# Kernel tuning notes

Hardware: AMD Instinct MI355X
Metric: run time of the kernel (lower is better)

The kernel has to match this reference:

```python
import jax, jax.numpy as jnp
import numpy as np
import math

NUM_BUCKETS = 32
MAX_DISTANCE = 128


def _relative_position_bucket(relative_position):
    # Unidirectional (bidirectional=False): rp = max(-relative_position, 0)
    rp = jnp.maximum(-relative_position, 0)
    max_exact = NUM_BUCKETS // 2  # 16
    is_small = rp < max_exact
    rp_f = jnp.maximum(rp, 1).astype(jnp.float32)
    large = max_exact + (
        jnp.log(rp_f / max_exact) / math.log(MAX_DISTANCE / max_exact)
        * (NUM_BUCKETS - max_exact)
    ).astype(jnp.int32)
    large = jnp.minimum(large, NUM_BUCKETS - 1)
    return jnp.where(is_small, rp, large)


def _t5_rel_bias(bias_table, T):
    # bias_table: [num_buckets, n_heads] -> [1, n_heads, T, T]
    ctx = jnp.arange(T, dtype=jnp.int32)[:, None]
    mem = jnp.arange(T, dtype=jnp.int32)[None, :]
    buckets = _relative_position_bucket(mem - ctx)  # [T, T]
    values = bias_table[buckets]  # [T, T, H]
    return jnp.transpose(values, (2, 0, 1))[None]  # [1, H, T, T]


def setup_inputs() -> dict:
    key = jax.random.key(0)
    ks = jax.random.split(key, 6)
    B, T, C, H = 2, 2048, 1024, 16
    x = jax.random.normal(ks[0], (B, T, C), dtype=jnp.float32)
    W_attn = jax.random.normal(ks[1], (C, 3 * C), dtype=jnp.float32) * 0.02
    b_attn = jnp.zeros((3 * C,), dtype=jnp.float32)
    W_proj = jax.random.normal(ks[2], (C, C), dtype=jnp.float32) * 0.02
    b_proj = jnp.zeros((C,), dtype=jnp.float32)
    bias_table = jax.random.normal(ks[3], (NUM_BUCKETS, H), dtype=jnp.float32) * 0.02
    return {"x": x, "W_attn": W_attn, "b_attn": b_attn,
            "W_proj": W_proj, "b_proj": b_proj, "bias_table": bias_table}


def reference(x, W_attn, b_attn, W_proj, b_proj, bias_table):
    B, T, C = x.shape
    H = bias_table.shape[1]
    D = C // H
    qkv = x @ W_attn + b_attn  # [B, T, 3C]
    q, k, v = jnp.split(qkv, 3, axis=-1)
    # [B, T, C] -> [B, H, T, D]
    q = q.reshape(B, T, H, D).transpose(0, 2, 1, 3)
    k = k.reshape(B, T, H, D).transpose(0, 2, 1, 3)
    v = v.reshape(B, T, H, D).transpose(0, 2, 1, 3)
    rel_bias = _t5_rel_bias(bias_table, T)  # [1, H, T, T]
    att = jnp.einsum('bhtd,bhsd->bhts', q, k) * (1.0 / math.sqrt(D))
    att = att + rel_bias
    causal = jnp.tril(jnp.ones((T, T), dtype=bool))
    att = jnp.where(causal, att, -jnp.inf)
    att = jax.nn.softmax(att, axis=-1)
    y = jnp.einsum('bhts,bhsd->bhtd', att, v)  # [B, H, T, D]
    y = y.transpose(0, 2, 1, 3).reshape(B, T, C)
    return y @ W_proj + b_proj
```

## Files before the change

kernel.cpp:

```cpp
#include <hip/hip_runtime.h>
#include <hip/hip_bf16.h>
#include <math.h>

typedef __attribute__((ext_vector_type(4))) float f32x4;
typedef __attribute__((ext_vector_type(16))) float f32x16;
typedef __attribute__((ext_vector_type(8))) __bf16 bf16x8;
typedef __attribute__((ext_vector_type(4))) __bf16 bf16x4;
typedef __attribute__((ext_vector_type(4))) unsigned int u32x4;
typedef __attribute__((ext_vector_type(2))) unsigned int u32x2;

#define DEVI __device__ __forceinline__

DEVI f32x4 mfma16(bf16x8 a, bf16x8 b, f32x4 c) {
  return __builtin_amdgcn_mfma_f32_16x16x32_bf16(a, b, c, 0, 0, 0);
}
DEVI f32x16 mfma32(bf16x8 a, bf16x8 b, f32x16 c) {
  return __builtin_amdgcn_mfma_f32_32x32x16_bf16(a, b, c, 0, 0, 0);
}

DEVI void gload16(const void* g, void* l) {
  __builtin_amdgcn_global_load_lds(
      (const __attribute__((address_space(1))) void*)g,
      (__attribute__((address_space(3))) void*)l, 16, 0, 0);
}

DEVI float exp2a(float x) {
  float r;
  asm("v_exp_f32 %0, %1" : "=v"(r) : "v"(x));
  return r;
}
DEVI unsigned cvtpk(float lo, float hi) {
  unsigned r;
  asm("v_cvt_pk_bf16_f32 %0, %1, %2" : "=v"(r) : "v"(lo), "v"(hi));
  return r;
}

#define LOG2E 1.4426950408889634f
#define QSCALE 0.18033688011110793f
#define FIXMAX 8.0f

__global__ __launch_bounds__(256) void prep_k(
    const float* __restrict__ x, const float* __restrict__ W_attn,
    const float* __restrict__ W_proj, const float* __restrict__ bt,
    __bf16* __restrict__ xb, __bf16* __restrict__ WaT,
    __bf16* __restrict__ WpT, float* __restrict__ tbl) {
  __shared__ float tile[32][33];
  int bid = blockIdx.x;
  const int t = threadIdx.x;
  if (bid < 4096) {
    int i = (bid * 256 + t) * 4;
    float4 v = *(const float4*)&x[i];
    bf16x4 o = {(__bf16)v.x, (__bf16)v.y, (__bf16)v.z, (__bf16)v.w};
    *(bf16x4*)&xb[i] = o;
    return;
  }
  bid -= 4096;
  if (bid < 4096) {
    const float* in;
    __bf16* out;
    int Cc, bx, by;
    if (bid < 3072) {
      in = W_attn; out = WaT; Cc = 3072; bx = bid % 96; by = bid / 96;
    } else {
      int b2 = bid - 3072;
      in = W_proj; out = WpT; Cc = 1024; bx = b2 % 32; by = b2 / 32;
    }
    const int R = 1024;
    int tx = t & 31, ty = t >> 5;
    int xcol = bx * 32 + tx;
    for (int r = ty; r < 32; r += 8)
      tile[r][tx] = in[(size_t)(by * 32 + r) * Cc + xcol];
    __syncthreads();
    int xo = by * 32 + tx;
    for (int r = ty; r < 32; r += 8)
      out[(size_t)(bx * 32 + r) * R + xo] = (__bf16)tile[tx][r];
    return;
  }
  bid -= 4096;
  int idx = bid * 256 + t;
  int h = idx >> 11, rp = idx & 2047;
  int bucket;
  if (rp < 16) {
    bucket = rp;
  } else {
    float v = (logf((float)rp * 0.0625f) / 2.0794415416798357f) * 16.0f;
    bucket = 16 + (int)v;
    if (bucket > 31) bucket = 31;
  }
  tbl[idx] = bt[bucket * 16 + h] * LOG2E;
}

template <int MODE>
__global__ __launch_bounds__(256) void gemm_bf16(
    const __bf16* __restrict__ A, const __bf16* __restrict__ BT,
    const float* __restrict__ bias, float* __restrict__ outF,
    __bf16* __restrict__ qb, __bf16* __restrict__ kb, __bf16* __restrict__ vtb,
    int M, int N, int K) {
  __shared__ __align__(16) __bf16 lA[2][128 * 32];
  __shared__ __align__(16) __bf16 lB[2][128 * 32];
  const int t = threadIdx.x;
  const int w = t >> 6, lane = t & 63;
  const int m0 = blockIdx.x * 128, n0 = blockIdx.y * 128;
  const int wr = (w >> 1) * 64, wc = (w & 1) * 64;

  f32x4 acc[4][4] = {};

  const int rA = lane & 15;
  const int kk = (lane >> 4) * 8;

  auto STAGE = [&](int buf, int k0) {
#pragma unroll
    for (int r = 0; r < 2; ++r) {
      int c = r * 256 + t;
      int row = c >> 2, cc = c & 3;
      gload16(A + (size_t)(m0 + row) * K + k0 + cc * 8,
              &lA[buf][(r * 256 + w * 64) * 8]);
      gload16(BT + (size_t)(n0 + row) * K + k0 + cc * 8,
              &lB[buf][(r * 256 + w * 64) * 8]);
    }
  };

  STAGE(0, 0);
  int cur = 0;
  for (int k0 = 0; k0 < K; k0 += 32, cur ^= 1) {
    __syncthreads();
    if (k0 + 32 < K) STAGE(cur ^ 1, k0 + 32);
    bf16x8 af[4], bfr[4];
#pragma unroll
    for (int i = 0; i < 4; ++i)
      af[i] = *(const bf16x8*)&lA[cur][(wr + i * 16 + rA) * 32 + kk];
#pragma unroll
    for (int j = 0; j < 4; ++j)
      bfr[j] = *(const bf16x8*)&lB[cur][(wc + j * 16 + rA) * 32 + kk];
#pragma unroll
    for (int i = 0; i < 4; ++i)
#pragma unroll
      for (int j = 0; j < 4; ++j)
        acc[i][j] = mfma16(af[i], bfr[j], acc[i][j]);
  }

  const int colb = n0 + wc + rA;
  const int rowb = m0 + wr + (lane >> 4) * 4;
#pragma unroll
  for (int j = 0; j < 4; ++j) {
    int n = colb + j * 16;
    float bv = bias[n];
#pragma unroll
    for (int i = 0; i < 4; ++i) {
#pragma unroll
      for (int e = 0; e < 4; ++e) {
        int m = rowb + i * 16 + e;
        float v = acc[i][j][e] + bv;
        if constexpr (MODE == 0) {
          int b = m >> 11, tt = m & 2047;
          int sec = n >> 10, nn = n & 1023;
          int h = nn >> 6, d = nn & 63;
          if (sec == 0)
            qb[(((size_t)(b * 16 + h)) * 2048 + tt) * 64 + d] = (__bf16)(v * QSCALE);
          else if (sec == 1)
            kb[(((size_t)(b * 16 + h)) * 2048 + tt) * 64 + d] = (__bf16)v;
          else
            vtb[(((size_t)(b * 16 + h)) * 64 + d) * 2048 + tt] = (__bf16)v;
        } else {
          outF[(size_t)m * N + n] = v;
        }
      }
    }
  }
}

__global__ __launch_bounds__(128) void attn_k(
    const __bf16* __restrict__ q, const __bf16* __restrict__ k,
    const __bf16* __restrict__ vt, const float* __restrict__ tbl,
    __bf16* __restrict__ y) {
  __shared__ __align__(16) __bf16 lK[64 * 64];
  __shared__ __align__(16) __bf16 lV[64 * 64];
  __shared__ float lb[128];

  const int t = threadIdx.x, w = t >> 6, lane = t & 63;
  const int bh = blockIdx.x, b = bh >> 4, h = bh & 15;
  const int qt = 31 - blockIdx.y;
  const int ncol = lane & 31, hi = lane >> 5;
  const int swl = ncol & 7;

  const __bf16* qp = q + (size_t)bh * 2048 * 64;
  const __bf16* kp = k + (size_t)bh * 2048 * 64;
  const __bf16* vp = vt + (size_t)bh * 64 * 2048;
  const float* tb = tbl + h * 2048;
  const float bconst = tb[2047] - FIXMAX;

  bf16x8 qf[4];
  {
    const __bf16* qr = qp + (size_t)(qt * 64 + w * 32 + ncol) * 64 + hi * 8;
#pragma unroll
    for (int dc = 0; dc < 4; ++dc) qf[dc] = *(const bf16x8*)(qr + dc * 16);
  }

  f32x16 O0 = {}, O1 = {};
  float lsum = 0.f;
  const int ib = 63 + 32 * w + ncol - 4 * hi;

  for (int jt = 0; jt <= qt; ++jt) {
    const int dt = qt - jt;
    __syncthreads();
#pragma unroll
    for (int i = 0; i < 4; ++i) {
      int id = i * 128 + t;
      int row = id >> 3, c = id & 7;
      int sc = c ^ (row & 7);
      gload16(kp + (size_t)(jt * 64 + row) * 64 + sc * 8,
              &lK[(i * 128 + w * 64) * 8]);
      gload16(vp + (size_t)row * 2048 + jt * 64 + sc * 8,
              &lV[(i * 128 + w * 64) * 8]);
    }
    if (dt < 3) {
      int rb2 = 64 * dt - 63 + t;
      lb[t] = tb[rb2 < 0 ? 0 : rb2] - FIXMAX;
    }
    __syncthreads();

#pragma unroll
    for (int kb = 0; kb < 2; ++kb) {
      const int rel = 2 * dt + w - kb;
      if (rel < 0) continue;

      f32x16 s;
      if (dt >= 3) {
#pragma unroll
        for (int r = 0; r < 16; ++r) s[r] = bconst;
      } else {
#pragma unroll
        for (int r = 0; r < 16; ++r) {
          int cr8 = (r & 3) + 8 * (r >> 2);
          float v = lb[ib - 32 * kb - cr8];
          if (rel == 0 && ncol < cr8 + 4 * hi) v = -1e30f;
          s[r] = v;
        }
      }
      const char* Kb = (const char*)lK + (kb * 32 + ncol) * 128;
#pragma unroll
      for (int dc = 0; dc < 4; ++dc) {
        bf16x8 kf = *(const bf16x8*)(Kb + (((dc * 2 + hi) ^ swl) << 4));
        s = mfma32(kf, qf[dc], s);
      }
      float p[16];
#pragma unroll
      for (int r = 0; r < 16; ++r) {
        p[r] = exp2a(s[r]);
        lsum += p[r];
      }
#pragma unroll
      for (int s16 = 0; s16 < 2; ++s16) {
        unsigned we0 = cvtpk(p[8 * s16 + 0], p[8 * s16 + 1]);
        unsigned we1 = cvtpk(p[8 * s16 + 2], p[8 * s16 + 3]);
        unsigned wo0 = cvtpk(p[8 * s16 + 4], p[8 * s16 + 5]);
        unsigned wo1 = cvtpk(p[8 * s16 + 6], p[8 * s16 + 7]);
        u32x2 r0 = __builtin_amdgcn_permlane32_swap(we0, wo0, false, false);
        u32x2 r1 = __builtin_amdgcn_permlane32_swap(we1, wo1, false, false);
        u32x4 aw = {r0[0], r1[0], r0[1], r1[1]};
        bf16x8 af = __builtin_bit_cast(bf16x8, aw);
#pragma unroll
        for (int db = 0; db < 2; ++db) {
          const char* Vb = (const char*)lV + (db * 32 + ncol) * 128;
          bf16x8 vf = *(const bf16x8*)(Vb +
              ((((kb * 2 + s16) * 2 + hi) ^ swl) << 4));
          if (db == 0) O0 = mfma32(af, vf, O0);
          else         O1 = mfma32(af, vf, O1);
        }
      }
    }
  }

  lsum += __shfl_xor(lsum, 32);
  float rinv = 1.0f / lsum;
#pragma unroll
  for (int r = 0; r < 16; ++r) {
    int cr = (r & 3) + 8 * (r >> 2) + 4 * hi;
    float ri = __shfl(rinv, cr);
    int row = qt * 64 + w * 32 + cr;
    size_t base = ((size_t)(b * 2048 + row)) * 1024 + h * 64 + ncol;
    y[base]      = (__bf16)(O0[r] * ri);
    y[base + 32] = (__bf16)(O1[r] * ri);
  }
}


extern "C" void kernel_launch(void* const* d_in, const int* in_sizes, int n_in,
                              void* d_out, int out_size, void* d_ws, size_t ws_size,
                              hipStream_t stream) {
  const float* x = (const float*)d_in[0];
  const float* W_attn = (const float*)d_in[1];
  const float* b_attn = (const float*)d_in[2];
  const float* W_proj = (const float*)d_in[3];
  const float* b_proj = (const float*)d_in[4];
  const float* bias_table = (const float*)d_in[5];
  float* out = (float*)d_out;

  char* ws = (char*)d_ws;
  __bf16* xb   = (__bf16*)(ws + 0);
  __bf16* WaT  = (__bf16*)(ws + 8388608);
  __bf16* WpT  = (__bf16*)(ws + 14680064);
  __bf16* qb   = (__bf16*)(ws + 16777216);
  __bf16* kb   = (__bf16*)(ws + 25165824);
  __bf16* vtb  = (__bf16*)(ws + 33554432);
  __bf16* yb   = (__bf16*)(ws + 41943040);
  float*  tbl  = (float*)(ws + 50331648);

  prep_k<<<8320, 256, 0, stream>>>(x, W_attn, W_proj, bias_table,
                                   xb, WaT, WpT, tbl);
  gemm_bf16<0><<<dim3(32, 24), 256, 0, stream>>>(xb, WaT, b_attn, nullptr,
                                                 qb, kb, vtb, 4096, 3072, 1024);
  attn_k<<<dim3(32, 32), 128, 0, stream>>>(qb, kb, vtb, tbl, yb);
  gemm_bf16<1><<<dim3(32, 8), 256, 0, stream>>>(yb, WpT, b_proj, out,
                                                nullptr, nullptr, nullptr,
                                                4096, 1024, 1024);
}
```

Measured before the change: 120.7 us.

## Split attention KV sub-tiles across four waves and double-buffer K/V loads

```diff
diff --git a/kernel.cpp b/kernel.cpp
--- a/kernel.cpp
+++ b/kernel.cpp
@@ -169,17 +169,17 @@
   }
 }
 
-__global__ __launch_bounds__(128) void attn_k(
+__global__ __launch_bounds__(256) void attn_k(
     const __bf16* __restrict__ q, const __bf16* __restrict__ k,
     const __bf16* __restrict__ vt, const float* __restrict__ tbl,
     __bf16* __restrict__ y) {
-  __shared__ __align__(16) __bf16 lK[64 * 64];
-  __shared__ __align__(16) __bf16 lV[64 * 64];
-  __shared__ float lb[128];
+  __shared__ __align__(16) char smem[2 * 8192 + 2 * 8192 + 2 * 768];
+  float* lbuf = (float*)(smem + 32768);
 
   const int t = threadIdx.x, w = t >> 6, lane = t & 63;
   const int bh = blockIdx.x, b = bh >> 4, h = bh & 15;
-  const int qt = 31 - blockIdx.y;
+  const int qt64 = 31 - blockIdx.y;
+  const int qs = w >> 1, ks = w & 1;
   const int ncol = lane & 31, hi = lane >> 5;
   const int swl = ncol & 7;
 
@@ -191,96 +191,130 @@
 
   bf16x8 qf[4];
   {
-    const __bf16* qr = qp + (size_t)(qt * 64 + w * 32 + ncol) * 64 + hi * 8;
+    const __bf16* qr = qp + (size_t)(qt64 * 64 + qs * 32 + ncol) * 64 + hi * 8;
 #pragma unroll
     for (int dc = 0; dc < 4; ++dc) qf[dc] = *(const bf16x8*)(qr + dc * 16);
   }
 
   f32x16 O0 = {}, O1 = {};
   float lsum = 0.f;
-  const int ib = 63 + 32 * w + ncol - 4 * hi;
-
-  for (int jt = 0; jt <= qt; ++jt) {
-    const int dt = qt - jt;
+  const int ibase = 95 + 32 * (qs - ks) - 4 * hi + ncol;
+
+  auto STAGE = [&](int buf, int jt) {
+#pragma unroll
+    for (int r = 0; r < 2; ++r) {
+      int c = r * 256 + t;
+      int row = c >> 3, cc = c & 7;
+      int sc = cc ^ (row & 7);
+      gload16(kp + (size_t)(jt * 64 + row) * 64 + sc * 8,
+              smem + buf * 8192 + (r * 256 + w * 64) * 16);
+      gload16(vp + (size_t)row * 2048 + jt * 64 + sc * 8,
+              smem + 16384 + buf * 8192 + (r * 256 + w * 64) * 16);
+    }
+    int dtj = qt64 - jt;
+    if (dtj < 3 && t < 192) {
+      int rb = dtj * 64 - 95 + t;
+      lbuf[buf * 192 + t] = tb[rb < 0 ? 0 : rb] - FIXMAX;
+    }
+  };
+
+  STAGE(0, 0);
+  int cur = 0;
+  for (int jt = 0; jt <= qt64; ++jt, cur ^= 1) {
+    const int dt = qt64 - jt;
+    const int rel = 2 * dt + qs - ks;
     __syncthreads();
-#pragma unroll
-    for (int i = 0; i < 4; ++i) {
-      int id = i * 128 + t;
-      int row = id >> 3, c = id & 7;
-      int sc = c ^ (row & 7);
-      gload16(kp + (size_t)(jt * 64 + row) * 64 + sc * 8,
-              &lK[(i * 128 + w * 64) * 8]);
-      gload16(vp + (size_t)row * 2048 + jt * 64 + sc * 8,
-              &lV[(i * 128 + w * 64) * 8]);
-    }
-    if (dt < 3) {
-      int rb2 = 64 * dt - 63 + t;
-      lb[t] = tb[rb2 < 0 ? 0 : rb2] - FIXMAX;
-    }
-    __syncthreads();
-
-#pragma unroll
-    for (int kb = 0; kb < 2; ++kb) {
-      const int rel = 2 * dt + w - kb;
-      if (rel < 0) continue;
-
-      f32x16 s;
-      if (dt >= 3) {
-#pragma unroll
-        for (int r = 0; r < 16; ++r) s[r] = bconst;
-      } else {
-#pragma unroll
-        for (int r = 0; r < 16; ++r) {
-          int cr8 = (r & 3) + 8 * (r >> 2);
-          float v = lb[ib - 32 * kb - cr8];
-          if (rel == 0 && ncol < cr8 + 4 * hi) v = -1e30f;
-          s[r] = v;
-        }
+    if (jt < qt64) STAGE(cur ^ 1, jt + 1);
+    if (rel < 0) continue;
+
+    const char* Kc = smem + cur * 8192;
+    const char* Vc = smem + 16384 + cur * 8192;
+    const float* lbc = lbuf + cur * 192;
+
+    f32x16 s;
+    if (rel >= 5) {
+#pragma unroll
+      for (int r = 0; r < 16; ++r) s[r] = bconst;
+    } else {
+#pragma unroll
+      for (int r = 0; r < 16; ++r) {
+        int cr8 = (r & 3) + 8 * (r >> 2);
+        float v = lbc[ibase - cr8];
+        if (rel == 0 && ncol < cr8 + 4 * hi) v = -1e30f;
+        s[r] = v;
       }
-      const char* Kb = (const char*)lK + (kb * 32 + ncol) * 128;
-#pragma unroll
-      for (int dc = 0; dc < 4; ++dc) {
-        bf16x8 kf = *(const bf16x8*)(Kb + (((dc * 2 + hi) ^ swl) << 4));
-        s = mfma32(kf, qf[dc], s);
+    }
+    const char* Kb = Kc + (ks * 32 + ncol) * 128;
+#pragma unroll
+    for (int dc = 0; dc < 4; ++dc) {
+      bf16x8 kf = *(const bf16x8*)(Kb + (((dc * 2 + hi) ^ swl) << 4));
+      s = mfma32(kf, qf[dc], s);
+    }
+    float p[16];
+#pragma unroll
+    for (int r = 0; r < 16; ++r) {
+      p[r] = exp2a(s[r]);
+      lsum += p[r];
+    }
+#pragma unroll
+    for (int s16 = 0; s16 < 2; ++s16) {
+      unsigned we0 = cvtpk(p[8 * s16 + 0], p[8 * s16 + 1]);
+      unsigned we1 = cvtpk(p[8 * s16 + 2], p[8 * s16 + 3]);
+      unsigned wo0 = cvtpk(p[8 * s16 + 4], p[8 * s16 + 5]);
+      unsigned wo1 = cvtpk(p[8 * s16 + 6], p[8 * s16 + 7]);
+      u32x2 r0 = __builtin_amdgcn_permlane32_swap(we0, wo0, false, false);
+      u32x2 r1 = __builtin_amdgcn_permlane32_swap(we1, wo1, false, false);
+      u32x4 aw = {r0[0], r1[0], r0[1], r1[1]};
+      bf16x8 af = __builtin_bit_cast(bf16x8, aw);
+#pragma unroll
+      for (int db = 0; db < 2; ++db) {
+        const char* Vb = Vc + (db * 32 + ncol) * 128;
+        bf16x8 vf = *(const bf16x8*)(Vb +
+            ((((ks * 2 + s16) * 2 + hi) ^ swl) << 4));
+        if (db == 0) O0 = mfma32(af, vf, O0);
+        else         O1 = mfma32(af, vf, O1);
       }
-      float p[16];
-#pragma unroll
-      for (int r = 0; r < 16; ++r) {
-        p[r] = exp2a(s[r]);
-        lsum += p[r];
+    }
+  }
+
+  lsum += __shfl_xor(lsum, 32);
+  __syncthreads();
+  float* ls = (float*)(smem + 32768);
+  if (ks) {
+    char* dst = smem + qs * 8192 + lane * 128;
+#pragma unroll
+    for (int c = 0; c < 4; ++c) {
+      f32x4 v0 = {O0[4 * c], O0[4 * c + 1], O0[4 * c + 2], O0[4 * c + 3]};
+      *(f32x4*)(dst + ((c ^ swl) << 4)) = v0;
+      f32x4 v1 = {O1[4 * c], O1[4 * c + 1], O1[4 * c + 2], O1[4 * c + 3]};
+      *(f32x4*)(dst + (((c + 4) ^ swl) << 4)) = v1;
+    }
+    ls[qs * 64 + lane] = lsum;
+  }
+  __syncthreads();
+  if (!ks) {
+    lsum += ls[qs * 64 + lane];
+    const char* src = smem + qs * 8192 + lane * 128;
+#pragma unroll
+    for (int c = 0; c < 4; ++c) {
+      f32x4 v0 = *(const f32x4*)(src + ((c ^ swl) << 4));
+      f32x4 v1 = *(const f32x4*)(src + (((c + 4) ^ swl) << 4));
+#pragma unroll
+      for (int e = 0; e < 4; ++e) {
+        O0[4 * c + e] += v0[e];
+        O1[4 * c + e] += v1[e];
       }
-#pragma unroll
-      for (int s16 = 0; s16 < 2; ++s16) {
-        unsigned we0 = cvtpk(p[8 * s16 + 0], p[8 * s16 + 1]);
-        unsigned we1 = cvtpk(p[8 * s16 + 2], p[8 * s16 + 3]);
-        unsigned wo0 = cvtpk(p[8 * s16 + 4], p[8 * s16 + 5]);
-        unsigned wo1 = cvtpk(p[8 * s16 + 6], p[8 * s16 + 7]);
-        u32x2 r0 = __builtin_amdgcn_permlane32_swap(we0, wo0, false, false);
-        u32x2 r1 = __builtin_amdgcn_permlane32_swap(we1, wo1, false, false);
-        u32x4 aw = {r0[0], r1[0], r0[1], r1[1]};
-        bf16x8 af = __builtin_bit_cast(bf16x8, aw);
-#pragma unroll
-        for (int db = 0; db < 2; ++db) {
-          const char* Vb = (const char*)lV + (db * 32 + ncol) * 128;
-          bf16x8 vf = *(const bf16x8*)(Vb +
-              ((((kb * 2 + s16) * 2 + hi) ^ swl) << 4));
-          if (db == 0) O0 = mfma32(af, vf, O0);
-          else         O1 = mfma32(af, vf, O1);
-        }
-      }
-    }
-  }
-
-  lsum += __shfl_xor(lsum, 32);
-  float rinv = 1.0f / lsum;
-#pragma unroll
-  for (int r = 0; r < 16; ++r) {
-    int cr = (r & 3) + 8 * (r >> 2) + 4 * hi;
-    float ri = __shfl(rinv, cr);
-    int row = qt * 64 + w * 32 + cr;
-    size_t base = ((size_t)(b * 2048 + row)) * 1024 + h * 64 + ncol;
-    y[base]      = (__bf16)(O0[r] * ri);
-    y[base + 32] = (__bf16)(O1[r] * ri);
+    }
+    float rinv = 1.0f / lsum;
+#pragma unroll
+    for (int r = 0; r < 16; ++r) {
+      int cr = (r & 3) + 8 * (r >> 2) + 4 * hi;
+      float ri = __shfl(rinv, cr);
+      int row = qt64 * 64 + qs * 32 + cr;
+      size_t base = ((size_t)(b * 2048 + row)) * 1024 + h * 64 + ncol;
+      y[base]      = (__bf16)(O0[r] * ri);
+      y[base + 32] = (__bf16)(O1[r] * ri);
+    }
   }
 }
 
@@ -310,7 +344,7 @@
                                    xb, WaT, WpT, tbl);
   gemm_bf16<0><<<dim3(32, 24), 256, 0, stream>>>(xb, WaT, b_attn, nullptr,
                                                  qb, kb, vtb, 4096, 3072, 1024);
-  attn_k<<<dim3(32, 32), 128, 0, stream>>>(qb, kb, vtb, tbl, yb);
+  attn_k<<<dim3(32, 32), 256, 0, stream>>>(qb, kb, vtb, tbl, yb);
   gemm_bf16<1><<<dim3(32, 8), 256, 0, stream>>>(yb, WpT, b_proj, out,
                                                 nullptr, nullptr, nullptr,
                                                 4096, 1024, 1024);
```

Measured after the change: 112.8 us. 6.6% less time.
